# Kernel tuning notes

Measured on AMD Instinct MI355X. Metric: run time of the kernel, lower is better.

Reference implementation:

```python
import jax, jax.numpy as jnp
import numpy as np

NUM_HEADS = 16
BN_EPS = 1e-5


def setup_inputs() -> dict:
    key = jax.random.key(0)
    ks = jax.random.split(key, 12)
    B, S, D = 8, 1024, 1024
    s = 1.0 / np.sqrt(D)
    return {
        "key": jax.random.normal(ks[0], (B, S, D), jnp.float32),
        "value": jax.random.normal(ks[1], (B, S, D), jnp.float32),
        "query": jax.random.normal(ks[2], (B, S, D), jnp.float32),
        "Wk": jax.random.normal(ks[3], (D, D), jnp.float32) * s,
        "bk": jax.random.normal(ks[4], (D,), jnp.float32) * s,
        "Wv": jax.random.normal(ks[5], (D, D), jnp.float32) * s,
        "bv": jax.random.normal(ks[6], (D,), jnp.float32) * s,
        "Wq": jax.random.normal(ks[7], (D, D), jnp.float32) * s,
        "bq": jax.random.normal(ks[8], (D,), jnp.float32) * s,
        "Wf": jax.random.normal(ks[9], (D, D), jnp.float32) * s,
        "bf": jax.random.normal(ks[10], (D,), jnp.float32) * s,
        "gamma": jnp.ones((D,), jnp.float32),
        "beta": jnp.zeros((D,), jnp.float32),
    }


def _mha(key, value, query, Wk, bk, Wv, bv, Wq, bq, Wf, bf, gamma, beta):
    B, S, D = query.shape
    H = NUM_HEADS
    d = D // H
    residual = query

    k = key @ Wk + bk      # [B, S, D]
    v = value @ Wv + bv
    q = query @ Wq + bq

    # Faithful to torch: raw row-major view(B*H, -1, d) — NOT the standard head transpose.
    k = k.reshape(B * H, -1, d)   # [B*H, S, d]
    v = v.reshape(B * H, -1, d)
    q = q.reshape(B * H, -1, d)

    # Faithful quirky scale: (dim_per_head // num_heads) ** -0.5
    scale = jnp.float32((d // H) ** (-0.5))

    scores = jnp.einsum('bqd,bkd->bqk', q, k) * scale          # [B*H, S, S]
    attention = jax.nn.softmax(scores, axis=2)
    context = jnp.einsum('bqk,bkd->bqd', attention, v)          # [B*H, S, d]

    context = context.reshape(B, -1, D)                         # [B, S, D]
    out = context @ Wf + bf

    # BatchNorm1d over channel dim D (training mode: batch stats over B and S, biased var)
    x = residual + out                                          # [B, S, D]
    mean = jnp.mean(x, axis=(0, 1))
    var = jnp.mean((x - mean) ** 2, axis=(0, 1))
    out = (x - mean) * jax.lax.rsqrt(var + BN_EPS) * gamma + beta
    return out, attention


def reference(key, value, query, Wk, bk, Wv, bv, Wq, bq, Wf, bf, gamma, beta):
    return _mha(key, value, query, Wk, bk, Wv, bv, Wq, bq, Wf, bf, gamma, beta)
```

## Files before the change

kernel.cpp:

```cpp
#include <hip/hip_runtime.h>
#include <hip/hip_bf16.h>
#include <stdint.h>

typedef __attribute__((ext_vector_type(8))) short     short8;
typedef __attribute__((ext_vector_type(8))) _Float16  f16x8;
typedef __attribute__((ext_vector_type(4))) float     f32x4;
typedef __attribute__((ext_vector_type(8))) unsigned short ushort8;
typedef __attribute__((ext_vector_type(4))) unsigned short ushort4_t;

__device__ inline unsigned short f2bf(float f) {
    unsigned u = __float_as_uint(f);
    u += 0x7fffu + ((u >> 16) & 1u);
    return (unsigned short)(u >> 16);
}
__device__ inline float bf2f(unsigned short h) {
    return __uint_as_float(((unsigned)h) << 16);
}
__device__ inline unsigned short f2h(float f) {
    _Float16 h = (_Float16)f;
    unsigned short r;
    __builtin_memcpy(&r, &h, 2);
    return r;
}

__device__ inline void gload16(const void* g, void* lds) {
    unsigned loff = (unsigned)(uintptr_t)lds;
    loff = __builtin_amdgcn_readfirstlane(loff);
    auto l = (__attribute__((address_space(3))) unsigned int*)(uintptr_t)loff;
    auto p = (const __attribute__((address_space(1))) unsigned int*)(uintptr_t)g;
    __builtin_amdgcn_global_load_lds(p, l, 16, 0, 0);
}

__global__ void cvt3_f32_2b(const float4* __restrict__ k, const float4* __restrict__ q,
                            const float4* __restrict__ v,
                            ushort4_t* __restrict__ k16, ushort4_t* __restrict__ q16,
                            ushort4_t* __restrict__ v16, int n4) {
    const int which = blockIdx.y;
    const float4* in  = which == 0 ? k   : which == 1 ? q   : v;
    ushort4_t*    out = which == 0 ? k16 : which == 1 ? q16 : v16;
    const bool tof16 = (which < 2);
    for (int i = blockIdx.x * blockDim.x + threadIdx.x; i < n4; i += gridDim.x * blockDim.x) {
        float4 vv = in[i];
        ushort4_t r;
        if (tof16) { r.x = f2h(vv.x);  r.y = f2h(vv.y);  r.z = f2h(vv.z);  r.w = f2h(vv.w); }
        else       { r.x = f2bf(vv.x); r.y = f2bf(vv.y); r.z = f2bf(vv.z); r.w = f2bf(vv.w); }
        out[i] = r;
    }
}

template<int TOF16>
__global__ void transpose_cvt(const float* __restrict__ W, unsigned short* __restrict__ WT, int dim) {
    __shared__ float t[32][33];
    const int bx = blockIdx.x * 32, by = blockIdx.y * 32;
    const int tx = threadIdx.x, ty = threadIdx.y;
#pragma unroll
    for (int i = 0; i < 4; ++i)
        t[ty + 8 * i][tx] = W[(size_t)(by + ty + 8 * i) * dim + bx + tx];
    __syncthreads();
#pragma unroll
    for (int i = 0; i < 4; ++i) {
        float v = t[tx][ty + 8 * i];
        WT[(size_t)(bx + ty + 8 * i) * dim + by + tx] = TOF16 ? f2h(v) : f2bf(v);
    }
}

__global__ void transpose_v(const unsigned short* __restrict__ v, unsigned short* __restrict__ vT) {
    const int bh = blockIdx.z, d0 = blockIdx.x * 32, s0 = blockIdx.y * 32;
    __shared__ unsigned short t[32][33];
    const int tx = threadIdx.x, ty = threadIdx.y;
    const size_t base = (size_t)bh << 16;
#pragma unroll
    for (int i = 0; i < 4; ++i)
        t[ty + 8 * i][tx] = v[base + (size_t)(s0 + ty + 8 * i) * 64 + d0 + tx];
    __syncthreads();
#pragma unroll
    for (int i = 0; i < 4; ++i)
        vT[base + (size_t)(d0 + ty + 8 * i) * 1024 + s0 + tx] = t[tx][ty + 8 * i];
}

template<int F16IN, int EPI>
__global__ __launch_bounds__(256, 2) void gemm_bt(
    const unsigned short* __restrict__ A,
    const unsigned short* __restrict__ Bt,
    const float* __restrict__ bias,
    unsigned short* __restrict__ C2b,
    const float* __restrict__ resid,
    float* __restrict__ Cf,
    int M, int N, int K, int nbx)
{
    const int bid = blockIdx.x;
    const int cpx = gridDim.x >> 3;
    const int swz = (bid & 7) * cpx + (bid >> 3);
    const int bm = swz / nbx, bn = swz % nbx;
    const int m0 = bm * 128, n0 = bn * 128;

    const int tid = threadIdx.x;
    const int w = tid >> 6, l = tid & 63, g = l >> 4, c = l & 15;
    const int wr = w >> 1, wc = w & 1;

    __shared__ unsigned short As[2][4096];
    __shared__ unsigned short Bs[2][4096];

    f32x4 acc[4][4] = {};

    const int arow = tid >> 2, acol = (tid & 3) * 8;
    const unsigned short* Ap  = A  + (size_t)(m0 + arow) * K + acol;
    const unsigned short* Ap2 = A  + (size_t)(m0 + 64 + arow) * K + acol;
    const unsigned short* Bp  = Bt + (size_t)(n0 + arow) * K + acol;
    const unsigned short* Bp2 = Bt + (size_t)(n0 + 64 + arow) * K + acol;

    const int NT = K >> 5;

#define STAGE_GEMM(bufi, koff)                                   \
    do {                                                         \
        gload16(Ap  + (koff), &As[bufi][w * 512]);               \
        gload16(Ap2 + (koff), &As[bufi][2048 + w * 512]);        \
        gload16(Bp  + (koff), &Bs[bufi][w * 512]);               \
        gload16(Bp2 + (koff), &Bs[bufi][2048 + w * 512]);        \
    } while (0)

#define COMPUTE_GEMM(bufi)                                                         \
    do {                                                                           \
        if constexpr (F16IN) {                                                     \
            f16x8 a[4], b[4];                                                      \
            _Pragma("unroll")                                                      \
            for (int mt = 0; mt < 4; ++mt)                                         \
                a[mt] = *(const f16x8*)&As[bufi][(wr * 64 + mt * 16 + c) * 32 + g * 8]; \
            _Pragma("unroll")                                                      \
            for (int nt = 0; nt < 4; ++nt)                                         \
                b[nt] = *(const f16x8*)&Bs[bufi][(wc * 64 + nt * 16 + c) * 32 + g * 8]; \
            _Pragma("unroll")                                                      \
            for (int mt = 0; mt < 4; ++mt)                                         \
                _Pragma("unroll")                                                  \
                for (int nt = 0; nt < 4; ++nt)                                     \
                    acc[mt][nt] = __builtin_amdgcn_mfma_f32_16x16x32_f16(a[mt], b[nt], acc[mt][nt], 0, 0, 0); \
        } else {                                                                   \
            short8 a[4], b[4];                                                     \
            _Pragma("unroll")                                                      \
            for (int mt = 0; mt < 4; ++mt)                                         \
                a[mt] = *(const short8*)&As[bufi][(wr * 64 + mt * 16 + c) * 32 + g * 8]; \
            _Pragma("unroll")                                                      \
            for (int nt = 0; nt < 4; ++nt)                                         \
                b[nt] = *(const short8*)&Bs[bufi][(wc * 64 + nt * 16 + c) * 32 + g * 8]; \
            _Pragma("unroll")                                                      \
            for (int mt = 0; mt < 4; ++mt)                                         \
                _Pragma("unroll")                                                  \
                for (int nt = 0; nt < 4; ++nt)                                     \
                    acc[mt][nt] = __builtin_amdgcn_mfma_f32_16x16x32_bf16(a[mt], b[nt], acc[mt][nt], 0, 0, 0); \
        }                                                                          \
    } while (0)

    STAGE_GEMM(0, 0);

#pragma unroll 2
    for (int kt = 0; kt < NT - 1; ++kt) {
        const int cur = kt & 1;
        STAGE_GEMM(cur ^ 1, (kt + 1) * 32);
        asm volatile("s_waitcnt vmcnt(4)" ::: "memory");
        __builtin_amdgcn_s_barrier();
        __builtin_amdgcn_sched_barrier(0);
        COMPUTE_GEMM(cur);
        __builtin_amdgcn_sched_barrier(0);
        __builtin_amdgcn_s_barrier();
    }
    asm volatile("s_waitcnt vmcnt(0)" ::: "memory");
    __builtin_amdgcn_s_barrier();
    __builtin_amdgcn_sched_barrier(0);
    COMPUTE_GEMM((NT - 1) & 1);

#undef STAGE_GEMM
#undef COMPUTE_GEMM

#pragma unroll
    for (int nt = 0; nt < 4; ++nt) {
        const int col = n0 + wc * 64 + nt * 16 + c;
        const float bs = bias[col];
#pragma unroll
        for (int mt = 0; mt < 4; ++mt) {
            const int row0 = m0 + wr * 64 + mt * 16 + g * 4;
#pragma unroll
            for (int r = 0; r < 4; ++r) {
                const float x = acc[mt][nt][r] + bs;
                const size_t idx = (size_t)(row0 + r) * N + col;
                if constexpr (EPI == 0) {
                    C2b[idx] = F16IN ? f2h(x) : f2bf(x);
                } else {
                    Cf[idx] = x + resid[idx];
                }
            }
        }
    }
}

__global__ __launch_bounds__(256, 4) void attn_kernel(
    const unsigned short* __restrict__ qf,
    const unsigned short* __restrict__ kf,
    const unsigned short* __restrict__ vT,
    float* __restrict__ attn_out,
    unsigned short* __restrict__ ctx)
{
    const int L = blockIdx.x;
    const int rb = (L >> 3) & 63;
    const int bh = ((L & 7) << 4) | (L >> 9);

    const int tid = threadIdx.x;
    const int w = tid >> 6, l = tid & 63, g = l >> 4, c = l & 15;
    const int n0 = w * 256;

    __shared__ unsigned short P[16 * 1024];
    __shared__ float rs_lds[4][16];
    __shared__ float inv_lds[16];

    const unsigned short* qb = qf + ((size_t)bh << 16) + (size_t)(rb * 16 + c) * 64 + g * 8;
    const f16x8 q0 = *(const f16x8*)(qb);
    const f16x8 q1 = *(const f16x8*)(qb + 32);

    const unsigned short* kb = kf + ((size_t)bh << 16);
    const unsigned swzc = ((unsigned)(c & 7)) << 4;
    const unsigned prow = (unsigned)c * 2048;

    ushort4_t pks[16];
    float rsum = 0.f;

#pragma unroll
    for (int t = 0; t < 16; ++t) {
        const unsigned short* kp = kb + (size_t)(n0 + t * 16 + c) * 64 + g * 8;
        const f16x8 a0 = *(const f16x8*)(kp);
        const f16x8 a1 = *(const f16x8*)(kp + 32);
        f32x4 s = {0.f, 0.f, 0.f, 0.f};
        s = __builtin_amdgcn_mfma_f32_16x16x32_f16(a0, q0, s, 0, 0, 0);
        s = __builtin_amdgcn_mfma_f32_16x16x32_f16(a1, q1, s, 0, 0, 0);

        const float p0 = __expf(s[0] * 0.5f);
        const float p1 = __expf(s[1] * 0.5f);
        const float p2 = __expf(s[2] * 0.5f);
        const float p3 = __expf(s[3] * 0.5f);
        rsum += (p0 + p1) + (p2 + p3);

        ushort4_t pk;
        pk.x = f2bf(p0); pk.y = f2bf(p1); pk.z = f2bf(p2); pk.w = f2bf(p3);
        pks[t] = pk;
        *(ushort4_t*)((char*)P + ((prow + (unsigned)(n0 * 2 + t * 32 + g * 8)) ^ swzc)) = pk;
    }

    rsum += __shfl_xor(rsum, 16);
    rsum += __shfl_xor(rsum, 32);
    if (g == 0) rs_lds[w][c] = rsum;
    __syncthreads();
    if (tid < 16)
        inv_lds[tid] = 1.0f / (rs_lds[0][tid] + rs_lds[1][tid] + rs_lds[2][tid] + rs_lds[3][tid]);
    __syncthreads();

    const float inv = inv_lds[c];
    float* ao = attn_out + ((size_t)bh << 20) + (size_t)(rb * 16 + c) * 1024 + n0 + g * 4;
    f32x4 pacc = {0.f, 0.f, 0.f, 0.f};
    const unsigned short* vb = vT + ((size_t)bh << 16) + (size_t)(w * 16 + c) * 1024;
#pragma unroll
    for (int ks = 0; ks < 32; ++ks) {
        const short8 a = *(const short8*)((char*)P + ((prow + (unsigned)(ks * 64 + g * 16)) ^ swzc));
        const short8 b = *(const short8*)(vb + ks * 32 + g * 8);
        pacc = __builtin_amdgcn_mfma_f32_16x16x32_bf16(a, b, pacc, 0, 0, 0);
        if (ks & 1) {
            const int t = ks >> 1;
            const ushort4_t pk = pks[t];
            f32x4 o;
            o[0] = bf2f(pk.x) * inv;
            o[1] = bf2f(pk.y) * inv;
            o[2] = bf2f(pk.z) * inv;
            o[3] = bf2f(pk.w) * inv;
            __builtin_nontemporal_store(o, (f32x4*)(ao + t * 16));
        }
    }
    unsigned short* cb = ctx + ((size_t)bh << 16) + (size_t)(rb * 16) * 64 + w * 16 + c;
#pragma unroll
    for (int r = 0; r < 4; ++r) {
        const int row = g * 4 + r;
        cb[(size_t)row * 64] = f2bf(pacc[r] * inv_lds[row]);
    }
}

__global__ void bn_stats(const float* __restrict__ x, float* __restrict__ psum, float* __restrict__ psq) {
    const int col = blockIdx.y * 256 + threadIdx.x;
    const int r0 = blockIdx.x * 128;
    float s = 0.f, q = 0.f;
#pragma unroll 4
    for (int r = 0; r < 128; ++r) {
        const float v = x[(size_t)(r0 + r) * 1024 + col];
        s += v; q += v * v;
    }
    psum[blockIdx.x * 1024 + col] = s;
    psq [blockIdx.x * 1024 + col] = q;
}

__global__ void bn_final(const float* __restrict__ psum, const float* __restrict__ psq,
                         const float* __restrict__ gamma, const float* __restrict__ beta,
                         float* __restrict__ ab) {
    const int cidx = threadIdx.x;
    float s = 0.f, q = 0.f;
#pragma unroll 8
    for (int i = 0; i < 64; ++i) { s += psum[i * 1024 + cidx]; q += psq[i * 1024 + cidx]; }
    const float mean = s * (1.0f / 8192.0f);
    const float var  = q * (1.0f / 8192.0f) - mean * mean;
    const float a = gamma[cidx] * rsqrtf(var + 1e-5f);
    ab[cidx]        = a;
    ab[1024 + cidx] = beta[cidx] - mean * a;
}

__global__ void bn_apply(const float4* __restrict__ x4, const float* __restrict__ ab, float4* __restrict__ o4) {
    const int n4 = 2 * 1024 * 1024;
    for (int i = blockIdx.x * blockDim.x + threadIdx.x; i < n4; i += gridDim.x * blockDim.x) {
        const float4 v = x4[i];
        const int c0 = (i & 255) << 2;
        float4 r;
        r.x = v.x * ab[c0 + 0] + ab[1024 + c0 + 0];
        r.y = v.y * ab[c0 + 1] + ab[1024 + c0 + 1];
        r.z = v.z * ab[c0 + 2] + ab[1024 + c0 + 2];
        r.w = v.w * ab[c0 + 3] + ab[1024 + c0 + 3];
        o4[i] = r;
    }
}

extern "C" void kernel_launch(void* const* d_in, const int* in_sizes, int n_in,
                              void* d_out, int out_size, void* d_ws, size_t ws_size,
                              hipStream_t stream) {
    (void)in_sizes; (void)n_in; (void)out_size; (void)ws_size;

    const float* key   = (const float*)d_in[0];
    const float* value = (const float*)d_in[1];
    const float* query = (const float*)d_in[2];
    const float* Wk = (const float*)d_in[3];
    const float* bk = (const float*)d_in[4];
    const float* Wv = (const float*)d_in[5];
    const float* bv = (const float*)d_in[6];
    const float* Wq = (const float*)d_in[7];
    const float* bq = (const float*)d_in[8];
    const float* Wf = (const float*)d_in[9];
    const float* bff = (const float*)d_in[10];
    const float* gamma = (const float*)d_in[11];
    const float* beta  = (const float*)d_in[12];

    char* ws = (char*)d_ws;
    const size_t MB = 1u << 20;
    unsigned short* key16   = (unsigned short*)(ws + 0);
    unsigned short* ctx     = (unsigned short*)(ws + 0);
    unsigned short* query16 = (unsigned short*)(ws + 16 * MB);
    unsigned short* value16 = (unsigned short*)(ws + 32 * MB);
    float*          xbuf    = (float*)(ws + 16 * MB);
    unsigned short* WkT = (unsigned short*)(ws + 48 * MB);
    unsigned short* WqT = (unsigned short*)(ws + 50 * MB);
    unsigned short* WvT = (unsigned short*)(ws + 52 * MB);
    unsigned short* WfT = (unsigned short*)(ws + 54 * MB);
    unsigned short* kbuf = (unsigned short*)(ws + 56 * MB);
    unsigned short* qbuf = (unsigned short*)(ws + 72 * MB);
    unsigned short* vbuf = (unsigned short*)(ws + 88 * MB);
    float* psum = (float*)(ws + 88 * MB);
    float* psq  = (float*)(ws + 88 * MB + 256 * 1024);
    float* ab   = (float*)(ws + 88 * MB + 512 * 1024);
    unsigned short* vTbuf = (unsigned short*)(ws + 104 * MB);

    float* out0 = (float*)d_out;
    float* attn = out0 + 8388608;

    const int n4big = 2 * 1024 * 1024;

    cvt3_f32_2b<<<dim3(1024, 3), 256, 0, stream>>>(
        (const float4*)key, (const float4*)query, (const float4*)value,
        (ushort4_t*)key16, (ushort4_t*)query16, (ushort4_t*)value16, n4big);

    dim3 tb(32, 8), tg(32, 32);
    transpose_cvt<1><<<tg, tb, 0, stream>>>(Wk, WkT, 1024);
    transpose_cvt<1><<<tg, tb, 0, stream>>>(Wq, WqT, 1024);
    transpose_cvt<0><<<tg, tb, 0, stream>>>(Wv, WvT, 1024);
    transpose_cvt<0><<<tg, tb, 0, stream>>>(Wf, WfT, 1024);

    gemm_bt<1, 0><<<512, 256, 0, stream>>>(key16,   WkT, bk, kbuf, nullptr, nullptr, 8192, 1024, 1024, 8);
    gemm_bt<1, 0><<<512, 256, 0, stream>>>(query16, WqT, bq, qbuf, nullptr, nullptr, 8192, 1024, 1024, 8);
    gemm_bt<0, 0><<<512, 256, 0, stream>>>(value16, WvT, bv, vbuf, nullptr, nullptr, 8192, 1024, 1024, 8);

    transpose_v<<<dim3(2, 32, 128), tb, 0, stream>>>(vbuf, vTbuf);

    attn_kernel<<<8192, 256, 0, stream>>>(qbuf, kbuf, vTbuf, attn, ctx);

    gemm_bt<0, 1><<<512, 256, 0, stream>>>(ctx, WfT, bff, nullptr, query, xbuf, 8192, 1024, 1024, 8);

    bn_stats<<<dim3(64, 4), 256, 0, stream>>>(xbuf, psum, psq);
    bn_final<<<1, 1024, 0, stream>>>(psum, psq, gamma, beta, ab);
    bn_apply<<<2048, 256, 0, stream>>>((const float4*)xbuf, ab, (float4*)out0);
}
```

Baseline: 445.6 us.

## Process 32 query rows per attention block, reusing K/V across two row tiles

Each attention block now handles 32 query rows instead of 16, so every K and V^T fragment loaded from memory feeds two MFMA tiles, and the grid shrinks to 4096 blocks. The score row is split into two 512-column halves so the shared P buffer keeps its size. The first half's P@V product is accumulated before the buffer is overwritten by the second half. This is meant to cut redundant K/V global/L2 traffic per query row, at the cost of twice the register-held P values, an extra barrier, and launch bounds lowered to two blocks per CU, which reduces occupancy.

```diff
diff --git a/kernel.cpp b/kernel.cpp
--- a/kernel.cpp
+++ b/kernel.cpp
@@ -192,7 +192,7 @@
     }
 }
 
-__global__ __launch_bounds__(256, 4) void attn_kernel(
+__global__ __launch_bounds__(256, 2) void attn_kernel(
     const unsigned short* __restrict__ qf,
     const unsigned short* __restrict__ kf,
     const unsigned short* __restrict__ vT,
@@ -200,82 +200,118 @@
     unsigned short* __restrict__ ctx)
 {
     const int L = blockIdx.x;
-    const int rb = (L >> 3) & 63;
-    const int bh = ((L & 7) << 4) | (L >> 9);
+    const int rb = (L >> 3) & 31;
+    const int bh = ((L & 7) << 4) | (L >> 8);
 
     const int tid = threadIdx.x;
     const int w = tid >> 6, l = tid & 63, g = l >> 4, c = l & 15;
-    const int n0 = w * 256;
-
-    __shared__ unsigned short P[16 * 1024];
-    __shared__ float rs_lds[4][16];
-    __shared__ float inv_lds[16];
-
-    const unsigned short* qb = qf + ((size_t)bh << 16) + (size_t)(rb * 16 + c) * 64 + g * 8;
-    const f16x8 q0 = *(const f16x8*)(qb);
-    const f16x8 q1 = *(const f16x8*)(qb + 32);
+
+    __shared__ unsigned short P[32 * 512];
+    __shared__ float rs_lds[4][32];
+    __shared__ float inv_lds[32];
+
+    const int rowA = c, rowB = 16 + c;
+    const unsigned short* qbase = qf + ((size_t)bh << 16) + (size_t)(rb * 32) * 64;
+    const f16x8 qA0 = *(const f16x8*)(qbase + (size_t)rowA * 64 + g * 8);
+    const f16x8 qA1 = *(const f16x8*)(qbase + (size_t)rowA * 64 + 32 + g * 8);
+    const f16x8 qB0 = *(const f16x8*)(qbase + (size_t)rowB * 64 + g * 8);
+    const f16x8 qB1 = *(const f16x8*)(qbase + (size_t)rowB * 64 + 32 + g * 8);
 
     const unsigned short* kb = kf + ((size_t)bh << 16);
     const unsigned swzc = ((unsigned)(c & 7)) << 4;
-    const unsigned prow = (unsigned)c * 2048;
-
-    ushort4_t pks[16];
-    float rsum = 0.f;
-
-#pragma unroll
-    for (int t = 0; t < 16; ++t) {
-        const unsigned short* kp = kb + (size_t)(n0 + t * 16 + c) * 64 + g * 8;
-        const f16x8 a0 = *(const f16x8*)(kp);
-        const f16x8 a1 = *(const f16x8*)(kp + 32);
-        f32x4 s = {0.f, 0.f, 0.f, 0.f};
-        s = __builtin_amdgcn_mfma_f32_16x16x32_f16(a0, q0, s, 0, 0, 0);
-        s = __builtin_amdgcn_mfma_f32_16x16x32_f16(a1, q1, s, 0, 0, 0);
-
-        const float p0 = __expf(s[0] * 0.5f);
-        const float p1 = __expf(s[1] * 0.5f);
-        const float p2 = __expf(s[2] * 0.5f);
-        const float p3 = __expf(s[3] * 0.5f);
-        rsum += (p0 + p1) + (p2 + p3);
-
-        ushort4_t pk;
-        pk.x = f2bf(p0); pk.y = f2bf(p1); pk.z = f2bf(p2); pk.w = f2bf(p3);
-        pks[t] = pk;
-        *(ushort4_t*)((char*)P + ((prow + (unsigned)(n0 * 2 + t * 32 + g * 8)) ^ swzc)) = pk;
-    }
-
-    rsum += __shfl_xor(rsum, 16);
-    rsum += __shfl_xor(rsum, 32);
-    if (g == 0) rs_lds[w][c] = rsum;
-    __syncthreads();
-    if (tid < 16)
+    const unsigned prowA = (unsigned)rowA * 1024;
+    const unsigned prowB = (unsigned)rowB * 1024;
+
+    ushort4_t pksA[16], pksB[16];
+    float rsumA = 0.f, rsumB = 0.f;
+    f32x4 paccA = {0.f, 0.f, 0.f, 0.f}, paccB = {0.f, 0.f, 0.f, 0.f};
+    const unsigned short* vb = vT + ((size_t)bh << 16) + (size_t)(w * 16 + c) * 1024;
+
+#define QKT_HALF(h)                                                              \
+    _Pragma("unroll")                                                            \
+    for (int t = 0; t < 8; ++t) {                                                \
+        const int col0 = (h) * 512 + w * 128 + t * 16;                           \
+        const unsigned short* kp = kb + (size_t)(col0 + c) * 64 + g * 8;         \
+        const f16x8 a0 = *(const f16x8*)(kp);                                    \
+        const f16x8 a1 = *(const f16x8*)(kp + 32);                               \
+        f32x4 sA = {0.f, 0.f, 0.f, 0.f}, sB = {0.f, 0.f, 0.f, 0.f};              \
+        sA = __builtin_amdgcn_mfma_f32_16x16x32_f16(a0, qA0, sA, 0, 0, 0);       \
+        sA = __builtin_amdgcn_mfma_f32_16x16x32_f16(a1, qA1, sA, 0, 0, 0);       \
+        sB = __builtin_amdgcn_mfma_f32_16x16x32_f16(a0, qB0, sB, 0, 0, 0);       \
+        sB = __builtin_amdgcn_mfma_f32_16x16x32_f16(a1, qB1, sB, 0, 0, 0);       \
+        ushort4_t pkA, pkB;                                                      \
+        { const float p0 = __expf(sA[0] * 0.5f), p1 = __expf(sA[1] * 0.5f);      \
+          const float p2 = __expf(sA[2] * 0.5f), p3 = __expf(sA[3] * 0.5f);      \
+          rsumA += (p0 + p1) + (p2 + p3);                                        \
+          pkA.x = f2bf(p0); pkA.y = f2bf(p1); pkA.z = f2bf(p2); pkA.w = f2bf(p3); } \
+        { const float p0 = __expf(sB[0] * 0.5f), p1 = __expf(sB[1] * 0.5f);      \
+          const float p2 = __expf(sB[2] * 0.5f), p3 = __expf(sB[3] * 0.5f);      \
+          rsumB += (p0 + p1) + (p2 + p3);                                        \
+          pkB.x = f2bf(p0); pkB.y = f2bf(p1); pkB.z = f2bf(p2); pkB.w = f2bf(p3); } \
+        pksA[(h) * 8 + t] = pkA;                                                 \
+        pksB[(h) * 8 + t] = pkB;                                                 \
+        const unsigned colb = (unsigned)(w * 256 + t * 32 + g * 8);              \
+        *(ushort4_t*)((char*)P + ((prowA + colb) ^ swzc)) = pkA;                 \
+        *(ushort4_t*)((char*)P + ((prowB + colb) ^ swzc)) = pkB;                 \
+    }
+
+#define PV_HALF(h, DO_STORE)                                                     \
+    _Pragma("unroll")                                                            \
+    for (int ks = 0; ks < 16; ++ks) {                                            \
+        const short8 aA = *(const short8*)((char*)P + ((prowA + (unsigned)(ks * 64 + g * 16)) ^ swzc)); \
+        const short8 aB = *(const short8*)((char*)P + ((prowB + (unsigned)(ks * 64 + g * 16)) ^ swzc)); \
+        const short8 b  = *(const short8*)(vb + (h) * 512 + ks * 32 + g * 8);    \
+        paccA = __builtin_amdgcn_mfma_f32_16x16x32_bf16(aA, b, paccA, 0, 0, 0);  \
+        paccB = __builtin_amdgcn_mfma_f32_16x16x32_bf16(aB, b, paccB, 0, 0, 0);  \
+        if (DO_STORE) {                                                          \
+            const int hh = ks >> 3, t2 = ks & 7;                                 \
+            const int col2 = hh * 512 + w * 128 + t2 * 16 + g * 4;               \
+            const ushort4_t pA = pksA[ks], pB = pksB[ks];                        \
+            f32x4 oA, oB;                                                        \
+            oA[0] = bf2f(pA.x) * invA; oA[1] = bf2f(pA.y) * invA;                \
+            oA[2] = bf2f(pA.z) * invA; oA[3] = bf2f(pA.w) * invA;                \
+            oB[0] = bf2f(pB.x) * invB; oB[1] = bf2f(pB.y) * invB;                \
+            oB[2] = bf2f(pB.z) * invB; oB[3] = bf2f(pB.w) * invB;                \
+            __builtin_nontemporal_store(oA, (f32x4*)(aoA + col2));               \
+            __builtin_nontemporal_store(oB, (f32x4*)(aoB + col2));               \
+        }                                                                        \
+    }
+
+    QKT_HALF(0)
+    __syncthreads();
+    { const float invA = 0.f, invB = 0.f; (void)invA; (void)invB;
+      float* aoA = nullptr; float* aoB = nullptr; (void)aoA; (void)aoB;
+      PV_HALF(0, 0) }
+    __syncthreads();
+    QKT_HALF(1)
+
+    rsumA += __shfl_xor(rsumA, 16);
+    rsumA += __shfl_xor(rsumA, 32);
+    rsumB += __shfl_xor(rsumB, 16);
+    rsumB += __shfl_xor(rsumB, 32);
+    if (g == 0) { rs_lds[w][c] = rsumA; rs_lds[w][16 + c] = rsumB; }
+    __syncthreads();
+    if (tid < 32)
         inv_lds[tid] = 1.0f / (rs_lds[0][tid] + rs_lds[1][tid] + rs_lds[2][tid] + rs_lds[3][tid]);
     __syncthreads();
 
-    const float inv = inv_lds[c];
-    float* ao = attn_out + ((size_t)bh << 20) + (size_t)(rb * 16 + c) * 1024 + n0 + g * 4;
-    f32x4 pacc = {0.f, 0.f, 0.f, 0.f};
-    const unsigned short* vb = vT + ((size_t)bh << 16) + (size_t)(w * 16 + c) * 1024;
-#pragma unroll
-    for (int ks = 0; ks < 32; ++ks) {
-        const short8 a = *(const short8*)((char*)P + ((prow + (unsigned)(ks * 64 + g * 16)) ^ swzc));
-        const short8 b = *(const short8*)(vb + ks * 32 + g * 8);
-        pacc = __builtin_amdgcn_mfma_f32_16x16x32_bf16(a, b, pacc, 0, 0, 0);
-        if (ks & 1) {
-            const int t = ks >> 1;
-            const ushort4_t pk = pks[t];
-            f32x4 o;
-            o[0] = bf2f(pk.x) * inv;
-            o[1] = bf2f(pk.y) * inv;
-            o[2] = bf2f(pk.z) * inv;
-            o[3] = bf2f(pk.w) * inv;
-            __builtin_nontemporal_store(o, (f32x4*)(ao + t * 16));
-        }
-    }
-    unsigned short* cb = ctx + ((size_t)bh << 16) + (size_t)(rb * 16) * 64 + w * 16 + c;
+    {
+        const float invA = inv_lds[rowA];
+        const float invB = inv_lds[rowB];
+        float* aoA = attn_out + ((size_t)bh << 20) + (size_t)(rb * 32 + rowA) * 1024;
+        float* aoB = attn_out + ((size_t)bh << 20) + (size_t)(rb * 32 + rowB) * 1024;
+        PV_HALF(1, 1)
+    }
+
+#undef QKT_HALF
+#undef PV_HALF
+
+    unsigned short* cb = ctx + ((size_t)bh << 16) + (size_t)(rb * 32) * 64 + w * 16 + c;
 #pragma unroll
     for (int r = 0; r < 4; ++r) {
-        const int row = g * 4 + r;
-        cb[(size_t)row * 64] = f2bf(pacc[r] * inv_lds[row]);
+        const int qrA = g * 4 + r, qrB = 16 + g * 4 + r;
+        cb[(size_t)qrA * 64] = f2bf(paccA[r] * inv_lds[qrA]);
+        cb[(size_t)qrB * 64] = f2bf(paccB[r] * inv_lds[qrB]);
     }
 }
 
@@ -379,7 +415,7 @@
 
     transpose_v<<<dim3(2, 32, 128), tb, 0, stream>>>(vbuf, vTbuf);
 
-    attn_kernel<<<8192, 256, 0, stream>>>(qbuf, kbuf, vTbuf, attn, ctx);
+    attn_kernel<<<4096, 256, 0, stream>>>(qbuf, kbuf, vTbuf, attn, ctx);
 
     gemm_bt<0, 1><<<512, 256, 0, stream>>>(ctx, WfT, bff, nullptr, query, xbuf, 8192, 1024, 1024, 8);
 
```

Result: slower. 514.8 us (+15.5%).
